# Kernel optimization log

Measured on AMD Instinct MI355X. Metric: run time of the kernel, lower is better.

The kernel has to match this reference:

```python
import jax, jax.numpy as jnp
import numpy as np

B, N, H, D, N_HEADS = 8, 2048, 1024, 1, 8
SCALE = H / N_HEADS  # 128.0 ; note: NOT sqrt, faithful to source


def _linear(x, w, b):
    # torch nn.Linear: y = x @ W^T + b ; w: [out, in]
    return jnp.einsum('bnh,oh->bno', x, w) + b


def setup_inputs() -> dict:
    key = jax.random.key(0)
    ks = jax.random.split(key, 18)
    s = 0.02
    inp = {
        'node_t': jax.random.normal(ks[0], (B, N, H), dtype=jnp.float32),
        'node_next': jax.random.normal(ks[1], (B, N, H), dtype=jnp.float32),
        'WQ_w': s * jax.random.normal(ks[2], (H, H), dtype=jnp.float32),
        'WQ_b': s * jax.random.normal(ks[3], (H,), dtype=jnp.float32),
        'WK_w': s * jax.random.normal(ks[4], (H, H), dtype=jnp.float32),
        'WK_b': s * jax.random.normal(ks[5], (H,), dtype=jnp.float32),
        'WV_w': s * jax.random.normal(ks[6], (H, H), dtype=jnp.float32),
        'WV_b': s * jax.random.normal(ks[7], (H,), dtype=jnp.float32),
        'WO_w': s * jax.random.normal(ks[8], (H, H), dtype=jnp.float32),
        'WO_b': s * jax.random.normal(ks[9], (H,), dtype=jnp.float32),
        'WE_w': s * jax.random.normal(ks[10], (H, H), dtype=jnp.float32),
        'WE_b': s * jax.random.normal(ks[11], (H,), dtype=jnp.float32),
        'WN_w': s * jax.random.normal(ks[12], (H, H), dtype=jnp.float32),
        'WN_b': s * jax.random.normal(ks[13], (H,), dtype=jnp.float32),
        'WA_w': s * jax.random.normal(ks[14], (D, H), dtype=jnp.float32),
        'WA_b': s * jax.random.normal(ks[15], (D,), dtype=jnp.float32),
    }
    return inp


def reference(node_t, node_next, WQ_w, WQ_b, WK_w, WK_b, WV_w, WV_b,
              WO_w, WO_b, WE_w, WE_b, WN_w, WN_b, WA_w, WA_b):
    Q = _linear(node_t, WQ_w, WQ_b)       # [B,N,H]
    K = _linear(node_next, WK_w, WK_b)    # [B,N,H]
    V = _linear(node_next, WV_w, WV_b)    # [B,N,H]
    att = jnp.einsum('bih,bkh->bik', Q, K)  # [B,N,N]
    # torch nn.Softmax() with no dim on a 3-D tensor -> legacy dim=0 (batch axis)
    att = jax.nn.softmax(att / SCALE, axis=0)
    # einsum('bnn,bnd->bnd') uses only the diagonal att[b,n,n]
    diag = jnp.einsum('bnn->bn', att)  # [B,N]
    av = diag[:, :, None] * V          # [B,N,H]
    h = jax.nn.gelu(_linear(av, WO_w, WO_b), approximate=False)  # exact erf GELU
    A_t = _linear(node_t, WE_w, WE_b) + _linear(h, WN_w, WN_b)   # [B,N,H]
    A_t = _linear(A_t, WA_w, WA_b)     # [B,N,1]
    return jnp.squeeze(A_t, axis=-1)   # [B,N]
```

## Files before the change

### kernel.cpp

```cpp
#include <hip/hip_runtime.h>
#include <cstdint>
#include <cstddef>


typedef __attribute__((ext_vector_type(8))) short bfx8;
typedef __attribute__((ext_vector_type(4))) short s16x4;
typedef __attribute__((ext_vector_type(4))) float f32x4;

#define N_SEQ 2048
#define M_TOT 16384
#define NT 16

__device__ __forceinline__ unsigned short f2bf(float f) {
  unsigned int u = __float_as_uint(f);
  return (unsigned short)((u + 0x7fffu + ((u >> 16) & 1u)) >> 16);
}
__device__ __forceinline__ float bf2f(short s) {
  return __uint_as_float(((unsigned int)(unsigned short)s) << 16);
}
__device__ __forceinline__ float gelu_exact(float g) {
  return 0.5f * g * (1.0f + erff(g * 0.70710678118654752f));
}
__device__ __forceinline__ void gload16(const void* g, void* l) {
  __builtin_amdgcn_global_load_lds(
      (const __attribute__((address_space(1))) unsigned int*)g,
      (__attribute__((address_space(3))) unsigned int*)(unsigned int)(uintptr_t)l,
      16, 0, 0);
}
__device__ __forceinline__ float dot4(float4 a, float4 b) {
  return a.x * b.x + a.y * b.y + a.z * b.z + a.w * b.w;
}

__global__ __launch_bounds__(256) void prep_w(
    const float* __restrict__ WQ, const float* __restrict__ WK,
    const float* __restrict__ WV, const float* __restrict__ WO,
    const float* __restrict__ WE, const float* __restrict__ WN,
    const float* __restrict__ wa, const float* __restrict__ bQ,
    const float* __restrict__ bK, const float* __restrict__ bV,
    const float* __restrict__ WEb, const float* __restrict__ WNb,
    const float* __restrict__ WAb,
    short* __restrict__ wqT, short* __restrict__ wkT,
    short* __restrict__ wvT, short* __restrict__ wo_bf,
    float* __restrict__ vE, float* __restrict__ vN,
    float* __restrict__ uQ, float* __restrict__ uK,
    float* __restrict__ c0, float* __restrict__ c1,
    float* __restrict__ bvw) {
  __shared__ short tile[64][65];
  __shared__ float redw[4];
  int bid = blockIdx.x, t = threadIdx.x;
  if (bid < 1024) {
    int z = bid >> 8, idx = bid & 255, bi = idx >> 4, bj = idx & 15;
    const float* src = z == 0 ? WQ : z == 1 ? WK : z == 2 ? WV : WO;
    if (z == 3) {
#pragma unroll
      for (int i = 0; i < 16; ++i) {
        int lin = i * 256 + t, r = lin >> 6, c = lin & 63;
        size_t idx2 = (size_t)(bi * 64 + r) * 1024 + bj * 64 + c;
        wo_bf[idx2] = (short)f2bf(src[idx2]);
      }
      return;
    }
    short* dst = z == 0 ? wqT : z == 1 ? wkT : wvT;
#pragma unroll
    for (int i = 0; i < 16; ++i) {
      int lin = i * 256 + t, r = lin >> 6, c = lin & 63;
      tile[r][c] = (short)f2bf(src[(size_t)(bi * 64 + r) * 1024 + bj * 64 + c]);
    }
    __syncthreads();
#pragma unroll
    for (int i = 0; i < 16; ++i) {
      int lin = i * 256 + t, r = lin >> 6, c = lin & 63;
      dst[(size_t)(bj * 64 + r) * 1024 + bi * 64 + c] = tile[c][r];
    }
  } else if (bid < 1280) {
    int idx = bid - 1024;
    int y = idx >> 6, ob = idx & 63;
    const float* M = y == 0 ? WE : y == 1 ? WN : y == 2 ? WQ : WK;
    const float* wv = (y < 2) ? wa : (y == 2 ? bK : bQ);
    float* dst = y == 0 ? vE : y == 1 ? vN : y == 2 ? uQ : uK;
    float a0 = 0.f, a1 = 0.f, a2 = 0.f, a3 = 0.f;
    int o0 = ob * 16;
#pragma unroll
    for (int i = 0; i < 16; ++i) {
      int o = o0 + i;
      float wvv = wv[o];
      const float* row = M + (size_t)o * 1024;
      a0 += wvv * row[t];
      a1 += wvv * row[t + 256];
      a2 += wvv * row[t + 512];
      a3 += wvv * row[t + 768];
    }
    atomicAdd(dst + t, a0);
    atomicAdd(dst + t + 256, a1);
    atomicAdd(dst + t + 512, a2);
    atomicAdd(dst + t + 768, a3);
  } else if (bid < 1282) {
    int which = bid - 1280;
    float a = 0.f;
    if (which == 0)
      for (int i = t; i < 1024; i += 256) a += wa[i] * (WEb[i] + WNb[i]);
    else
      for (int i = t; i < 1024; i += 256) a += bQ[i] * bK[i];
#pragma unroll
    for (int o = 32; o > 0; o >>= 1) a += __shfl_down(a, o, 64);
    if ((t & 63) == 0) redw[t >> 6] = a;
    __syncthreads();
    if (t == 0) {
      float tot = redw[0] + redw[1] + redw[2] + redw[3];
      if (which == 0) c0[0] = tot + WAb[0];
      else c1[0] = tot;
    }
  } else {
    int r = bid - 1282;
    float4 wv = ((const float4*)(WO + (size_t)r * 1024))[t];
    float4 bv = ((const float4*)bV)[t];
    float a = dot4(wv, bv);
#pragma unroll
    for (int o = 32; o > 0; o >>= 1) a += __shfl_down(a, o, 64);
    if ((t & 63) == 0) redw[t >> 6] = a;
    __syncthreads();
    if (t == 0) bvw[r] = redw[0] + redw[1] + redw[2] + redw[3];
  }
}

__global__ __launch_bounds__(256) void prep2(
    const short* __restrict__ wqT, const short* __restrict__ wkT,
    const short* __restrict__ wvT, const short* __restrict__ wo_bf,
    short* __restrict__ M1, short* __restrict__ M2,
    const float* __restrict__ nn, const float* __restrict__ uK,
    short* __restrict__ xn, float* __restrict__ xk) {
  __shared__ short sA[128 * 64];
  __shared__ short sB[128 * 64];
  int bid = blockIdx.x, tid = threadIdx.x;
  if (bid >= 128) {
    int lane = tid & 63, wv = tid >> 6;
    int idx = bid - 128;
    const float4* v4 = (const float4*)uK + lane * 4;
    float4 u0 = v4[0], u1 = v4[1], u2 = v4[2], u3 = v4[3];
    int row = idx * 8 + wv * 2;
#pragma unroll
    for (int rr = 0; rr < 2; ++rr) {
      const float4* src = (const float4*)(nn + (size_t)(row + rr) * 1024)
                          + lane * 4;
      float4 a0 = src[0], a1 = src[1], a2 = src[2], a3 = src[3];
      bfx8 o0, o1;
      o0[0] = (short)f2bf(a0.x); o0[1] = (short)f2bf(a0.y);
      o0[2] = (short)f2bf(a0.z); o0[3] = (short)f2bf(a0.w);
      o0[4] = (short)f2bf(a1.x); o0[5] = (short)f2bf(a1.y);
      o0[6] = (short)f2bf(a1.z); o0[7] = (short)f2bf(a1.w);
      o1[0] = (short)f2bf(a2.x); o1[1] = (short)f2bf(a2.y);
      o1[2] = (short)f2bf(a2.z); o1[3] = (short)f2bf(a2.w);
      o1[4] = (short)f2bf(a3.x); o1[5] = (short)f2bf(a3.y);
      o1[6] = (short)f2bf(a3.z); o1[7] = (short)f2bf(a3.w);
      bfx8* dst = (bfx8*)(xn + (size_t)(row + rr) * 1024 + lane * 16);
      dst[0] = o0; dst[1] = o1;
      float a = dot4(a0, u0) + dot4(a1, u1) + dot4(a2, u2) + dot4(a3, u3);
#pragma unroll
      for (int o = 32; o > 0; o >>= 1) a += __shfl_xor(a, o, 64);
      if (lane == 0) xk[row + rr] = a;
    }
    return;
  }
  int z = bid >> 6, by = (bid >> 3) & 7, bx = bid & 7;
  const short* A = z ? wo_bf : wqT;
  const short* B = z ? wvT : wkT;
  short* D = z ? M2 : M1;
  int lane = tid & 63, w = tid >> 6;
  int wm = w >> 1, wn = w & 1;
  f32x4 acc[4][4] = {};
  int lrow = lane & 15, lk = (lane >> 4) * 8;
  int srow = lane >> 3, scol = (lane & 7) * 8;
  const short* Ag = A + (size_t)by * 128 * 1024;
  const short* Bg = B + (size_t)bx * 128 * 1024;
  for (int k0 = 0; k0 < 1024; k0 += 64) {
#pragma unroll
    for (int i = 0; i < 4; ++i) {
      int c = w * 4 + i;
      gload16(Ag + (size_t)(c * 8 + srow) * 1024 + k0 + scol, sA + c * 512);
      gload16(Bg + (size_t)(c * 8 + srow) * 1024 + k0 + scol, sB + c * 512);
    }
    __syncthreads();
#pragma unroll
    for (int kk = 0; kk < 64; kk += 32) {
      bfx8 af[4], bfr[4];
#pragma unroll
      for (int mi = 0; mi < 4; ++mi)
        af[mi] = *(const bfx8*)(sA + (wm * 64 + mi * 16 + lrow) * 64 + kk + lk);
#pragma unroll
      for (int nj = 0; nj < 4; ++nj)
        bfr[nj] = *(const bfx8*)(sB + (wn * 64 + nj * 16 + lrow) * 64 + kk + lk);
#pragma unroll
      for (int mi = 0; mi < 4; ++mi)
#pragma unroll
        for (int nj = 0; nj < 4; ++nj)
          acc[mi][nj] = __builtin_amdgcn_mfma_f32_16x16x32_bf16(
              af[mi], bfr[nj], acc[mi][nj], 0, 0, 0);
    }
    __syncthreads();
  }
  int r0 = by * 128 + wm * 64, cb2 = bx * 128 + wn * 64;
#pragma unroll
  for (int mi = 0; mi < 4; ++mi)
#pragma unroll
    for (int nj = 0; nj < 4; ++nj) {
      int col = cb2 + nj * 16 + lrow;
#pragma unroll
      for (int r = 0; r < 4; ++r) {
        int row = r0 + mi * 16 + (lane >> 4) * 4 + r;
        D[(size_t)row * 1024 + col] = (short)f2bf(acc[mi][nj][r]);
      }
    }
}

__global__ __launch_bounds__(256, 2) void gemm_main(
    const short* __restrict__ A, const short* __restrict__ Bf,
    const float* __restrict__ bias2, const float* __restrict__ nodet,
    const float* __restrict__ vE, float* __restrict__ xe,
    float* __restrict__ sPart, short* __restrict__ vw) {
  __shared__ short sA[2][8192];
  __shared__ short sB[2][8192];
  int tid = threadIdx.x;
  if (blockIdx.x >= 2048) {
    int lane = tid & 63, wv2 = tid >> 6;
    int idx = blockIdx.x - 2048;
    const float4* v4 = (const float4*)vE + lane * 4;
    float4 u0 = v4[0], u1 = v4[1], u2 = v4[2], u3 = v4[3];
    int row = idx * 8 + wv2 * 2;
#pragma unroll
    for (int rr = 0; rr < 2; ++rr) {
      const float4* src = (const float4*)(nodet + (size_t)(row + rr) * 1024)
                          + lane * 4;
      float4 a0 = src[0], a1 = src[1], a2 = src[2], a3 = src[3];
      float a = dot4(a0, u0) + dot4(a1, u1) + dot4(a2, u2) + dot4(a3, u3);
#pragma unroll
      for (int o = 32; o > 0; o >>= 1) a += __shfl_xor(a, o, 64);
      if (lane == 0) xe[row + rr] = a;
    }
    return;
  }
  int lane = tid & 63, w = tid >> 6;
  int wm = w >> 1, wn = w & 1;
  int wg = blockIdx.x;
  int xcd = wg & 7, sub = wg >> 3;
  int tt = sub >> 4, within = sub & 15;
  int by = xcd * 16 + (tt >> 2) * 4 + (within >> 2);
  int bx = (tt & 3) * 4 + (within & 3);
  int lrow = lane & 15, g = lane >> 4;
  int sw0 = g ^ (lrow & 7);
  int sg = (lane & 7) ^ (lane >> 3);
  const short* Agt = A + ((size_t)(by * 128 + w * 32 + (lane >> 3))) * 1024 + sg * 8;
  const short* Bgt = Bf + ((size_t)(bx * 128 + w * 32 + (lane >> 3))) * 1024 + sg * 8;

  f32x4 acc[4][4] = {};

  auto stage = [&](int buf, int kt) {
    const short* ag = Agt + kt * 64;
    const short* bg = Bgt + kt * 64;
    short* la = &sA[buf][w * 2048];
    short* lb = &sB[buf][w * 2048];
#pragma unroll
    for (int i = 0; i < 4; ++i) {
      gload16(ag + i * 8192, la + i * 512);
      gload16(bg + i * 8192, lb + i * 512);
    }
  };

  stage(0, 0);
  int cur = 0;
  int arow = wm * 64 + lrow, brow = wn * 64 + lrow;
  for (int kt = 0; kt < NT; ++kt) {
    if (kt + 1 < NT) {
      stage(cur ^ 1, kt + 1);
      asm volatile("s_waitcnt vmcnt(8)" ::: "memory");
    } else {
      asm volatile("s_waitcnt vmcnt(0)" ::: "memory");
    }
    __builtin_amdgcn_sched_barrier(0);
    __builtin_amdgcn_s_barrier();
    __builtin_amdgcn_sched_barrier(0);

    const short* sa = &sA[cur][0];
    const short* sb = &sB[cur][0];
    bfx8 bq[4][2];
#pragma unroll
    for (int nj = 0; nj < 4; ++nj) {
      bq[nj][0] = *(const bfx8*)(sb + (brow + nj * 16) * 64 + sw0 * 8);
      bq[nj][1] = *(const bfx8*)(sb + (brow + nj * 16) * 64 + (sw0 ^ 4) * 8);
    }
#pragma unroll
    for (int q = 0; q < 2; ++q) {
      bfx8 a00 = *(const bfx8*)(sa + (arow + (2 * q) * 16) * 64 + sw0 * 8);
      bfx8 a01 = *(const bfx8*)(sa + (arow + (2 * q) * 16) * 64 + (sw0 ^ 4) * 8);
      bfx8 a10 = *(const bfx8*)(sa + (arow + (2 * q + 1) * 16) * 64 + sw0 * 8);
      bfx8 a11 = *(const bfx8*)(sa + (arow + (2 * q + 1) * 16) * 64 + (sw0 ^ 4) * 8);
      __builtin_amdgcn_s_setprio(1);
#pragma unroll
      for (int nj = 0; nj < 4; ++nj) {
        acc[2 * q][nj] = __builtin_amdgcn_mfma_f32_16x16x32_bf16(
            a00, bq[nj][0], acc[2 * q][nj], 0, 0, 0);
        acc[2 * q][nj] = __builtin_amdgcn_mfma_f32_16x16x32_bf16(
            a01, bq[nj][1], acc[2 * q][nj], 0, 0, 0);
        acc[2 * q + 1][nj] = __builtin_amdgcn_mfma_f32_16x16x32_bf16(
            a10, bq[nj][0], acc[2 * q + 1][nj], 0, 0, 0);
        acc[2 * q + 1][nj] = __builtin_amdgcn_mfma_f32_16x16x32_bf16(
            a11, bq[nj][1], acc[2 * q + 1][nj], 0, 0, 0);
      }
      __builtin_amdgcn_s_setprio(0);
    }
    __builtin_amdgcn_sched_barrier(0);
    __builtin_amdgcn_s_barrier();
    __builtin_amdgcn_sched_barrier(0);
    cur ^= 1;
  }

  int row0 = by * 128 + wm * 64;
  int cb = bx * 128 + wn * 64;
  if (bx < 8) {
    float bias_nj[4];
#pragma unroll
    for (int nj = 0; nj < 4; ++nj) bias_nj[nj] = bias2[cb + nj * 16 + lrow];
    int px = bx * 2 + wn;
#pragma unroll
    for (int mi = 0; mi < 4; ++mi) {
#pragma unroll
      for (int r = 0; r < 4; ++r) {
        int row = row0 + mi * 16 + g * 4 + r;
        const float* xr = nodet + (size_t)row * 1024;
        float v = 0.f;
#pragma unroll
        for (int nj = 0; nj < 4; ++nj)
          v += (acc[mi][nj][r] + bias_nj[nj]) * xr[cb + nj * 16 + lrow];
        v += __shfl_xor(v, 1, 64);
        v += __shfl_xor(v, 2, 64);
        v += __shfl_xor(v, 4, 64);
        v += __shfl_xor(v, 8, 64);
        if (lrow == 0) sPart[(size_t)row * 16 + px] = v;
      }
    }
  } else {
#pragma unroll
    for (int mi = 0; mi < 4; ++mi)
#pragma unroll
      for (int nj = 0; nj < 4; ++nj) {
        int colv = cb - 1024 + nj * 16 + lrow;
        float bv = bias2[1024 + colv];
#pragma unroll
        for (int r = 0; r < 4; ++r) {
          int row = row0 + mi * 16 + g * 4 + r;
          vw[(size_t)row * 1024 + colv] = (short)f2bf(acc[mi][nj][r] + bv);
        }
      }
  }
}

__global__ __launch_bounds__(512) void out2_kernel(
    const short* __restrict__ vw, const float* __restrict__ sPart,
    const float* __restrict__ xe, const float* __restrict__ xk,
    const float* __restrict__ vN, const float* __restrict__ bO,
    const float* __restrict__ c0p, const float* __restrict__ c1p,
    float* __restrict__ out) {
  int n = blockIdx.x, t = threadIdx.x;
  __shared__ float sS[8];
  if (t < 128) {
    int b = t >> 4, j = t & 15;
    size_t row = (size_t)b * N_SEQ + n;
    float p = sPart[row * 16 + j];
    p += __shfl_xor(p, 1, 64);
    p += __shfl_xor(p, 2, 64);
    p += __shfl_xor(p, 4, 64);
    p += __shfl_xor(p, 8, 64);
    if (j == 0) sS[b] = p + xk[row] + c1p[0];
  }
  __syncthreads();
  int b = t >> 6, lane = t & 63;
  float m = sS[0];
#pragma unroll
  for (int i = 1; i < 8; ++i) m = fmaxf(m, sS[i]);
  float sum = 0.f, eb = 0.f;
#pragma unroll
  for (int i = 0; i < 8; ++i) {
    float e = expf((sS[i] - m) * (1.0f / 128.0f));
    sum += e;
    if (i == b) eb = e;
  }
  float d = eb / sum;
  size_t row = (size_t)b * N_SEQ + n;
  const s16x4* vv = (const s16x4*)(vw + row * 1024 + lane * 16);
  const float4* bo4 = (const float4*)bO + lane * 4;
  const float4* vn4 = (const float4*)vN + lane * 4;
  float a = 0.f;
#pragma unroll
  for (int q = 0; q < 4; ++q) {
    s16x4 v = vv[q];
    float4 bo = bo4[q], vn = vn4[q];
    float gx;
    gx = fmaf(d, bf2f(v[0]), bo.x); a += gelu_exact(gx) * vn.x;
    gx = fmaf(d, bf2f(v[1]), bo.y); a += gelu_exact(gx) * vn.y;
    gx = fmaf(d, bf2f(v[2]), bo.z); a += gelu_exact(gx) * vn.z;
    gx = fmaf(d, bf2f(v[3]), bo.w); a += gelu_exact(gx) * vn.w;
  }
#pragma unroll
  for (int o = 32; o > 0; o >>= 1) a += __shfl_xor(a, o, 64);
  if (lane == 0) out[row] = xe[row] + c0p[0] + a;
}

extern "C" void kernel_launch(void* const* d_in, const int* in_sizes, int n_in,
                              void* d_out, int out_size, void* d_ws,
                              size_t ws_size, hipStream_t stream) {
  const float* nt  = (const float*)d_in[0];
  const float* nn  = (const float*)d_in[1];
  const float* WQ  = (const float*)d_in[2];
  const float* bQ  = (const float*)d_in[3];
  const float* WK  = (const float*)d_in[4];
  const float* bK  = (const float*)d_in[5];
  const float* WV  = (const float*)d_in[6];
  const float* bV  = (const float*)d_in[7];
  const float* WO  = (const float*)d_in[8];
  const float* bO  = (const float*)d_in[9];
  const float* WE  = (const float*)d_in[10];
  const float* WEb = (const float*)d_in[11];
  const float* WN  = (const float*)d_in[12];
  const float* WNb = (const float*)d_in[13];
  const float* wa  = (const float*)d_in[14];
  const float* WAb = (const float*)d_in[15];
  float* out = (float*)d_out;

  char* w = (char*)d_ws;
  size_t o = 0;
  const size_t BIG = (size_t)M_TOT * 1024 * 2;
  short* xn     = (short*)(w + o); o += BIG;
  short* vw     = (short*)(w + o); o += BIG;
  short* Bf     = (short*)(w + o); o += (size_t)2048 * 1024 * 2;
  short* wqT    = (short*)(w + o); o += 2097152;
  short* wkT    = (short*)(w + o); o += 2097152;
  short* wvT    = (short*)(w + o); o += 2097152;
  short* wo_bf  = (short*)(w + o); o += 2097152;
  float* sPart  = (float*)(w + o); o += (size_t)M_TOT * 16 * 4;
  float* bias2  = (float*)(w + o); o += 8192;
  float* vE     = (float*)(w + o); o += 4096;
  float* vN     = (float*)(w + o); o += 4096;
  float* uK     = (float*)(w + o); o += 4096;
  float* xk     = (float*)(w + o); o += 65536;
  float* xe     = (float*)(w + o); o += 65536;
  float* c0     = (float*)(w + o); o += 256;
  float* c1     = (float*)(w + o); o += 256;
  (void)ws_size; (void)in_sizes; (void)n_in; (void)out_size;

  hipMemsetAsync(bias2, 0, 8192 + 4096 * 3, stream);

  prep_w<<<2306, 256, 0, stream>>>(WQ, WK, WV, WO, WE, WN, wa, bQ, bK, bV,
                                   WEb, WNb, WAb, wqT, wkT, wvT, wo_bf,
                                   vE, vN, bias2, uK, c0, c1, bias2 + 1024);
  prep2<<<2176, 256, 0, stream>>>(wqT, wkT, wvT, wo_bf, Bf, Bf + 1048576,
                                  nn, uK, xn, xk);
  gemm_main<<<4096, 256, 0, stream>>>(xn, Bf, bias2, nt, vE, xe, sPart, vw);
  out2_kernel<<<N_SEQ, 512, 0, stream>>>(vw, sPart, xe, xk, vN, bO,
                                         c0, c1, out);
}
```

Measured before the change: 153.2 us.

## Rebalance work across prep kernels and shrink weight-product GEMM tiles

Moves the fp32-to-bf16 conversion of node_next into prep_w, moves the xe row-dot (node_t·vE) out of gemm_main into prep2, and computes xk from the bf16 copy instead of fp32. The prep2 weight-product GEMM switches from 128x128 to 64x64 tiles, giving 512 blocks instead of 128 for better CU fill. gemm_main drops its extra blocks and uses a simpler XCD-interleaved tile mapping. The aim is to shorten the serial prep kernels and fill the GPU better, at the cost of less data reuse in the smaller tiles and a slightly different xk precision.

```diff
diff --git a/kernel.cpp b/kernel.cpp
--- a/kernel.cpp
+++ b/kernel.cpp
@@ -38,106 +38,19 @@
     const float* __restrict__ wa, const float* __restrict__ bQ,
     const float* __restrict__ bK, const float* __restrict__ bV,
     const float* __restrict__ WEb, const float* __restrict__ WNb,
-    const float* __restrict__ WAb,
+    const float* __restrict__ WAb, const float* __restrict__ nn,
     short* __restrict__ wqT, short* __restrict__ wkT,
     short* __restrict__ wvT, short* __restrict__ wo_bf,
     float* __restrict__ vE, float* __restrict__ vN,
     float* __restrict__ uQ, float* __restrict__ uK,
     float* __restrict__ c0, float* __restrict__ c1,
-    float* __restrict__ bvw) {
+    float* __restrict__ bvw, short* __restrict__ xn) {
   __shared__ short tile[64][65];
   __shared__ float redw[4];
   int bid = blockIdx.x, t = threadIdx.x;
-  if (bid < 1024) {
-    int z = bid >> 8, idx = bid & 255, bi = idx >> 4, bj = idx & 15;
-    const float* src = z == 0 ? WQ : z == 1 ? WK : z == 2 ? WV : WO;
-    if (z == 3) {
-#pragma unroll
-      for (int i = 0; i < 16; ++i) {
-        int lin = i * 256 + t, r = lin >> 6, c = lin & 63;
-        size_t idx2 = (size_t)(bi * 64 + r) * 1024 + bj * 64 + c;
-        wo_bf[idx2] = (short)f2bf(src[idx2]);
-      }
-      return;
-    }
-    short* dst = z == 0 ? wqT : z == 1 ? wkT : wvT;
-#pragma unroll
-    for (int i = 0; i < 16; ++i) {
-      int lin = i * 256 + t, r = lin >> 6, c = lin & 63;
-      tile[r][c] = (short)f2bf(src[(size_t)(bi * 64 + r) * 1024 + bj * 64 + c]);
-    }
-    __syncthreads();
-#pragma unroll
-    for (int i = 0; i < 16; ++i) {
-      int lin = i * 256 + t, r = lin >> 6, c = lin & 63;
-      dst[(size_t)(bj * 64 + r) * 1024 + bi * 64 + c] = tile[c][r];
-    }
-  } else if (bid < 1280) {
-    int idx = bid - 1024;
-    int y = idx >> 6, ob = idx & 63;
-    const float* M = y == 0 ? WE : y == 1 ? WN : y == 2 ? WQ : WK;
-    const float* wv = (y < 2) ? wa : (y == 2 ? bK : bQ);
-    float* dst = y == 0 ? vE : y == 1 ? vN : y == 2 ? uQ : uK;
-    float a0 = 0.f, a1 = 0.f, a2 = 0.f, a3 = 0.f;
-    int o0 = ob * 16;
-#pragma unroll
-    for (int i = 0; i < 16; ++i) {
-      int o = o0 + i;
-      float wvv = wv[o];
-      const float* row = M + (size_t)o * 1024;
-      a0 += wvv * row[t];
-      a1 += wvv * row[t + 256];
-      a2 += wvv * row[t + 512];
-      a3 += wvv * row[t + 768];
-    }
-    atomicAdd(dst + t, a0);
-    atomicAdd(dst + t + 256, a1);
-    atomicAdd(dst + t + 512, a2);
-    atomicAdd(dst + t + 768, a3);
-  } else if (bid < 1282) {
-    int which = bid - 1280;
-    float a = 0.f;
-    if (which == 0)
-      for (int i = t; i < 1024; i += 256) a += wa[i] * (WEb[i] + WNb[i]);
-    else
-      for (int i = t; i < 1024; i += 256) a += bQ[i] * bK[i];
-#pragma unroll
-    for (int o = 32; o > 0; o >>= 1) a += __shfl_down(a, o, 64);
-    if ((t & 63) == 0) redw[t >> 6] = a;
-    __syncthreads();
-    if (t == 0) {
-      float tot = redw[0] + redw[1] + redw[2] + redw[3];
-      if (which == 0) c0[0] = tot + WAb[0];
-      else c1[0] = tot;
-    }
-  } else {
-    int r = bid - 1282;
-    float4 wv = ((const float4*)(WO + (size_t)r * 1024))[t];
-    float4 bv = ((const float4*)bV)[t];
-    float a = dot4(wv, bv);
-#pragma unroll
-    for (int o = 32; o > 0; o >>= 1) a += __shfl_down(a, o, 64);
-    if ((t & 63) == 0) redw[t >> 6] = a;
-    __syncthreads();
-    if (t == 0) bvw[r] = redw[0] + redw[1] + redw[2] + redw[3];
-  }
-}
-
-__global__ __launch_bounds__(256) void prep2(
-    const short* __restrict__ wqT, const short* __restrict__ wkT,
-    const short* __restrict__ wvT, const short* __restrict__ wo_bf,
-    short* __restrict__ M1, short* __restrict__ M2,
-    const float* __restrict__ nn, const float* __restrict__ uK,
-    short* __restrict__ xn, float* __restrict__ xk) {
-  __shared__ short sA[128 * 64];
-  __shared__ short sB[128 * 64];
-  int bid = blockIdx.x, tid = threadIdx.x;
-  if (bid >= 128) {
-    int lane = tid & 63, wv = tid >> 6;
-    int idx = bid - 128;
-    const float4* v4 = (const float4*)uK + lane * 4;
-    float4 u0 = v4[0], u1 = v4[1], u2 = v4[2], u3 = v4[3];
-    int row = idx * 8 + wv * 2;
+  if (bid >= 2306) {
+    int lane = t & 63, wv = t >> 6;
+    int row = (bid - 2306) * 8 + wv * 2;
 #pragma unroll
     for (int rr = 0; rr < 2; ++rr) {
       const float4* src = (const float4*)(nn + (size_t)(row + rr) * 1024)
@@ -154,55 +67,176 @@
       o1[6] = (short)f2bf(a3.z); o1[7] = (short)f2bf(a3.w);
       bfx8* dst = (bfx8*)(xn + (size_t)(row + rr) * 1024 + lane * 16);
       dst[0] = o0; dst[1] = o1;
-      float a = dot4(a0, u0) + dot4(a1, u1) + dot4(a2, u2) + dot4(a3, u3);
+    }
+    return;
+  }
+  if (bid < 1024) {
+    int z = bid >> 8, idx = bid & 255, bi = idx >> 4, bj = idx & 15;
+    const float* src = z == 0 ? WQ : z == 1 ? WK : z == 2 ? WV : WO;
+    if (z == 3) {
+#pragma unroll
+      for (int i = 0; i < 16; ++i) {
+        int lin = i * 256 + t, r = lin >> 6, c = lin & 63;
+        size_t idx2 = (size_t)(bi * 64 + r) * 1024 + bj * 64 + c;
+        wo_bf[idx2] = (short)f2bf(src[idx2]);
+      }
+      return;
+    }
+    short* dst = z == 0 ? wqT : z == 1 ? wkT : wvT;
+#pragma unroll
+    for (int i = 0; i < 16; ++i) {
+      int lin = i * 256 + t, r = lin >> 6, c = lin & 63;
+      tile[r][c] = (short)f2bf(src[(size_t)(bi * 64 + r) * 1024 + bj * 64 + c]);
+    }
+    __syncthreads();
+#pragma unroll
+    for (int i = 0; i < 16; ++i) {
+      int lin = i * 256 + t, r = lin >> 6, c = lin & 63;
+      dst[(size_t)(bj * 64 + r) * 1024 + bi * 64 + c] = tile[c][r];
+    }
+  } else if (bid < 1280) {
+    int idx = bid - 1024;
+    int y = idx >> 6, ob = idx & 63;
+    const float* M = y == 0 ? WE : y == 1 ? WN : y == 2 ? WQ : WK;
+    const float* wv = (y < 2) ? wa : (y == 2 ? bK : bQ);
+    float* dst = y == 0 ? vE : y == 1 ? vN : y == 2 ? uQ : uK;
+    float a0 = 0.f, a1 = 0.f, a2 = 0.f, a3 = 0.f;
+    int o0 = ob * 16;
+#pragma unroll
+    for (int i = 0; i < 16; ++i) {
+      int o = o0 + i;
+      float wvv = wv[o];
+      const float* row = M + (size_t)o * 1024;
+      a0 += wvv * row[t];
+      a1 += wvv * row[t + 256];
+      a2 += wvv * row[t + 512];
+      a3 += wvv * row[t + 768];
+    }
+    atomicAdd(dst + t, a0);
+    atomicAdd(dst + t + 256, a1);
+    atomicAdd(dst + t + 512, a2);
+    atomicAdd(dst + t + 768, a3);
+  } else if (bid < 1282) {
+    int which = bid - 1280;
+    float a = 0.f;
+    if (which == 0)
+      for (int i = t; i < 1024; i += 256) a += wa[i] * (WEb[i] + WNb[i]);
+    else
+      for (int i = t; i < 1024; i += 256) a += bQ[i] * bK[i];
+#pragma unroll
+    for (int o = 32; o > 0; o >>= 1) a += __shfl_down(a, o, 64);
+    if ((t & 63) == 0) redw[t >> 6] = a;
+    __syncthreads();
+    if (t == 0) {
+      float tot = redw[0] + redw[1] + redw[2] + redw[3];
+      if (which == 0) c0[0] = tot + WAb[0];
+      else c1[0] = tot;
+    }
+  } else {
+    int r = bid - 1282;
+    float4 wv = ((const float4*)(WO + (size_t)r * 1024))[t];
+    float4 bv = ((const float4*)bV)[t];
+    float a = dot4(wv, bv);
+#pragma unroll
+    for (int o = 32; o > 0; o >>= 1) a += __shfl_down(a, o, 64);
+    if ((t & 63) == 0) redw[t >> 6] = a;
+    __syncthreads();
+    if (t == 0) bvw[r] = redw[0] + redw[1] + redw[2] + redw[3];
+  }
+}
+
+__global__ __launch_bounds__(256) void prep2(
+    const short* __restrict__ wqT, const short* __restrict__ wkT,
+    const short* __restrict__ wvT, const short* __restrict__ wo_bf,
+    short* __restrict__ M1, short* __restrict__ M2,
+    const float* __restrict__ nt, const float* __restrict__ vE,
+    const float* __restrict__ uK, const short* __restrict__ xn,
+    float* __restrict__ xe, float* __restrict__ xk) {
+  __shared__ short sA[64 * 64];
+  __shared__ short sB[64 * 64];
+  int bid = blockIdx.x, tid = threadIdx.x;
+  if (bid >= 2560) {
+    int lane = tid & 63, wv = tid >> 6;
+    int row = (bid - 2560) * 8 + wv * 2;
+    const float4* u4 = (const float4*)uK + lane * 4;
+    float4 u0 = u4[0], u1 = u4[1], u2 = u4[2], u3 = u4[3];
+#pragma unroll
+    for (int rr = 0; rr < 2; ++rr) {
+      const bfx8* src = (const bfx8*)(xn + (size_t)(row + rr) * 1024 + lane * 16);
+      bfx8 b0 = src[0], b1 = src[1];
+      float a = bf2f(b0[0]) * u0.x + bf2f(b0[1]) * u0.y +
+                bf2f(b0[2]) * u0.z + bf2f(b0[3]) * u0.w +
+                bf2f(b0[4]) * u1.x + bf2f(b0[5]) * u1.y +
+                bf2f(b0[6]) * u1.z + bf2f(b0[7]) * u1.w +
+                bf2f(b1[0]) * u2.x + bf2f(b1[1]) * u2.y +
+                bf2f(b1[2]) * u2.z + bf2f(b1[3]) * u2.w +
+                bf2f(b1[4]) * u3.x + bf2f(b1[5]) * u3.y +
+                bf2f(b1[6]) * u3.z + bf2f(b1[7]) * u3.w;
 #pragma unroll
       for (int o = 32; o > 0; o >>= 1) a += __shfl_xor(a, o, 64);
       if (lane == 0) xk[row + rr] = a;
     }
     return;
   }
-  int z = bid >> 6, by = (bid >> 3) & 7, bx = bid & 7;
+  if (bid >= 512) {
+    int lane = tid & 63, wv = tid >> 6;
+    int row = (bid - 512) * 8 + wv * 2;
+    const float4* v4 = (const float4*)vE + lane * 4;
+    float4 u0 = v4[0], u1 = v4[1], u2 = v4[2], u3 = v4[3];
+#pragma unroll
+    for (int rr = 0; rr < 2; ++rr) {
+      const float4* src = (const float4*)(nt + (size_t)(row + rr) * 1024)
+                          + lane * 4;
+      float a = dot4(src[0], u0) + dot4(src[1], u1) +
+                dot4(src[2], u2) + dot4(src[3], u3);
+#pragma unroll
+      for (int o = 32; o > 0; o >>= 1) a += __shfl_xor(a, o, 64);
+      if (lane == 0) xe[row + rr] = a;
+    }
+    return;
+  }
+  int z = bid >> 8, by = (bid >> 4) & 15, bx = bid & 15;
   const short* A = z ? wo_bf : wqT;
   const short* B = z ? wvT : wkT;
   short* D = z ? M2 : M1;
   int lane = tid & 63, w = tid >> 6;
   int wm = w >> 1, wn = w & 1;
-  f32x4 acc[4][4] = {};
+  f32x4 acc[2][2] = {};
   int lrow = lane & 15, lk = (lane >> 4) * 8;
   int srow = lane >> 3, scol = (lane & 7) * 8;
-  const short* Ag = A + (size_t)by * 128 * 1024;
-  const short* Bg = B + (size_t)bx * 128 * 1024;
+  const short* Ag = A + (size_t)by * 64 * 1024;
+  const short* Bg = B + (size_t)bx * 64 * 1024;
   for (int k0 = 0; k0 < 1024; k0 += 64) {
 #pragma unroll
-    for (int i = 0; i < 4; ++i) {
-      int c = w * 4 + i;
+    for (int i = 0; i < 2; ++i) {
+      int c = w * 2 + i;
       gload16(Ag + (size_t)(c * 8 + srow) * 1024 + k0 + scol, sA + c * 512);
       gload16(Bg + (size_t)(c * 8 + srow) * 1024 + k0 + scol, sB + c * 512);
     }
     __syncthreads();
 #pragma unroll
     for (int kk = 0; kk < 64; kk += 32) {
-      bfx8 af[4], bfr[4];
-#pragma unroll
-      for (int mi = 0; mi < 4; ++mi)
-        af[mi] = *(const bfx8*)(sA + (wm * 64 + mi * 16 + lrow) * 64 + kk + lk);
-#pragma unroll
-      for (int nj = 0; nj < 4; ++nj)
-        bfr[nj] = *(const bfx8*)(sB + (wn * 64 + nj * 16 + lrow) * 64 + kk + lk);
-#pragma unroll
-      for (int mi = 0; mi < 4; ++mi)
-#pragma unroll
-        for (int nj = 0; nj < 4; ++nj)
+      bfx8 af[2], bfr[2];
+#pragma unroll
+      for (int mi = 0; mi < 2; ++mi)
+        af[mi] = *(const bfx8*)(sA + (wm * 32 + mi * 16 + lrow) * 64 + kk + lk);
+#pragma unroll
+      for (int nj = 0; nj < 2; ++nj)
+        bfr[nj] = *(const bfx8*)(sB + (wn * 32 + nj * 16 + lrow) * 64 + kk + lk);
+#pragma unroll
+      for (int mi = 0; mi < 2; ++mi)
+#pragma unroll
+        for (int nj = 0; nj < 2; ++nj)
           acc[mi][nj] = __builtin_amdgcn_mfma_f32_16x16x32_bf16(
               af[mi], bfr[nj], acc[mi][nj], 0, 0, 0);
     }
     __syncthreads();
   }
-  int r0 = by * 128 + wm * 64, cb2 = bx * 128 + wn * 64;
-#pragma unroll
-  for (int mi = 0; mi < 4; ++mi)
-#pragma unroll
-    for (int nj = 0; nj < 4; ++nj) {
+  int r0 = by * 64 + wm * 32, cb2 = bx * 64 + wn * 32;
+#pragma unroll
+  for (int mi = 0; mi < 2; ++mi)
+#pragma unroll
+    for (int nj = 0; nj < 2; ++nj) {
       int col = cb2 + nj * 16 + lrow;
 #pragma unroll
       for (int r = 0; r < 4; ++r) {
@@ -215,36 +249,15 @@
 __global__ __launch_bounds__(256, 2) void gemm_main(
     const short* __restrict__ A, const short* __restrict__ Bf,
     const float* __restrict__ bias2, const float* __restrict__ nodet,
-    const float* __restrict__ vE, float* __restrict__ xe,
     float* __restrict__ sPart, short* __restrict__ vw) {
   __shared__ short sA[2][8192];
   __shared__ short sB[2][8192];
   int tid = threadIdx.x;
-  if (blockIdx.x >= 2048) {
-    int lane = tid & 63, wv2 = tid >> 6;
-    int idx = blockIdx.x - 2048;
-    const float4* v4 = (const float4*)vE + lane * 4;
-    float4 u0 = v4[0], u1 = v4[1], u2 = v4[2], u3 = v4[3];
-    int row = idx * 8 + wv2 * 2;
-#pragma unroll
-    for (int rr = 0; rr < 2; ++rr) {
-      const float4* src = (const float4*)(nodet + (size_t)(row + rr) * 1024)
-                          + lane * 4;
-      float4 a0 = src[0], a1 = src[1], a2 = src[2], a3 = src[3];
-      float a = dot4(a0, u0) + dot4(a1, u1) + dot4(a2, u2) + dot4(a3, u3);
-#pragma unroll
-      for (int o = 32; o > 0; o >>= 1) a += __shfl_xor(a, o, 64);
-      if (lane == 0) xe[row + rr] = a;
-    }
-    return;
-  }
   int lane = tid & 63, w = tid >> 6;
   int wm = w >> 1, wn = w & 1;
   int wg = blockIdx.x;
-  int xcd = wg & 7, sub = wg >> 3;
-  int tt = sub >> 4, within = sub & 15;
-  int by = xcd * 16 + (tt >> 2) * 4 + (within >> 2);
-  int bx = (tt & 3) * 4 + (within & 3);
+  int work = (wg & 7) * 256 + (wg >> 3);
+  int by = work >> 4, bx = work & 15;
   int lrow = lane & 15, g = lane >> 4;
   int sw0 = g ^ (lrow & 7);
   int sg = (lane & 7) ^ (lane >> 3);
@@ -448,12 +461,13 @@
 
   hipMemsetAsync(bias2, 0, 8192 + 4096 * 3, stream);
 
-  prep_w<<<2306, 256, 0, stream>>>(WQ, WK, WV, WO, WE, WN, wa, bQ, bK, bV,
-                                   WEb, WNb, WAb, wqT, wkT, wvT, wo_bf,
-                                   vE, vN, bias2, uK, c0, c1, bias2 + 1024);
-  prep2<<<2176, 256, 0, stream>>>(wqT, wkT, wvT, wo_bf, Bf, Bf + 1048576,
-                                  nn, uK, xn, xk);
-  gemm_main<<<4096, 256, 0, stream>>>(xn, Bf, bias2, nt, vE, xe, sPart, vw);
+  prep_w<<<4354, 256, 0, stream>>>(WQ, WK, WV, WO, WE, WN, wa, bQ, bK, bV,
+                                   WEb, WNb, WAb, nn, wqT, wkT, wvT, wo_bf,
+                                   vE, vN, bias2, uK, c0, c1, bias2 + 1024,
+                                   xn);
+  prep2<<<4608, 256, 0, stream>>>(wqT, wkT, wvT, wo_bf, Bf, Bf + 1048576,
+                                  nt, vE, uK, xn, xe, xk);
+  gemm_main<<<2048, 256, 0, stream>>>(xn, Bf, bias2, nt, sPart, vw);
   out2_kernel<<<N_SEQ, 512, 0, stream>>>(vw, sPart, xe, xk, vN, bO,
                                          c0, c1, out);
 }
```

Result: slower. 156.3 us (+2.0%).
